# Kernel tuning notes

Hardware: AMD Instinct MI355X
Metric: run time of the kernel (lower is better)

Reference implementation:

```python
import jax, jax.numpy as jnp
import numpy as np

B, S, D, H = 2, 2048, 1024, 16
DK = D // H

def setup_inputs() -> dict:
    key = jax.random.key(0)
    ks = jax.random.split(key, 11)
    scale = 1.0 / np.sqrt(D)
    inp = {
        'q': jax.random.normal(ks[0], (B, S, D), jnp.float32),
        'k': jax.random.normal(ks[1], (B, S, D), jnp.float32),
        'v': jax.random.normal(ks[2], (B, S, D), jnp.float32),
        'Wq': jax.random.normal(ks[3], (D, D), jnp.float32) * scale,
        'bq': jnp.zeros((D,), jnp.float32),
        'Wk': jax.random.normal(ks[4], (D, D), jnp.float32) * scale,
        'bk': jnp.zeros((D,), jnp.float32),
        'Wv': jax.random.normal(ks[5], (D, D), jnp.float32) * scale,
        'bv': jnp.zeros((D,), jnp.float32),
        'Wo': jax.random.normal(ks[6], (D, D), jnp.float32) * scale,
        'bo': jnp.zeros((D,), jnp.float32),
    }
    return inp

def reference(q, k, v, Wq, bq, Wk, bk, Wv, bv, Wo, bo):
    # linear projections
    qp = q @ Wq + bq   # [B,S,D]
    kp = k @ Wk + bk
    vp = v @ Wv + bv
    # split heads -> [B,H,S,DK]
    qh = qp.reshape(B, S, H, DK).transpose(0, 2, 1, 3)
    kh = kp.reshape(B, S, H, DK).transpose(0, 2, 1, 3)
    vh = vp.reshape(B, S, H, DK).transpose(0, 2, 1, 3)
    scaled = jnp.einsum('bhqd,bhkd->bhqk', qh, kh) / jnp.sqrt(jnp.float32(DK))
    attn_score = jax.nn.softmax(scaled, axis=-1)  # [B,H,S,S]
    x = jnp.einsum('bhqk,bhkd->bhqd', attn_score, vh)
    # dropout is identity in eval mode
    out = x.transpose(0, 2, 1, 3).reshape(B, S, D)
    return (out @ Wo + bo, attn_score)
```

## Files before the change

kernel.cpp:

```cpp
#include <hip/hip_runtime.h>
#include <hip/hip_bf16.h>
#include <stdint.h>
#include <stddef.h>

typedef unsigned short u16;
typedef __attribute__((ext_vector_type(8))) short short8;
typedef __attribute__((ext_vector_type(4))) short bfx4;
typedef __attribute__((ext_vector_type(4))) float f32x4;
typedef __attribute__((ext_vector_type(4))) float f4;

constexpr int B_ = 2, S_ = 2048, D_ = 1024, H_ = 16;
constexpr size_t OUT_ELEMS = (size_t)B_ * S_ * D_;

__device__ __forceinline__ u16 f2bf(float f) {
    union { float f; unsigned u; } v; v.f = f;
    unsigned r = 0x7FFFu + ((v.u >> 16) & 1u);
    return (u16)((v.u + r) >> 16);
}

__device__ __forceinline__ void gload16(const void* g, void* l) {
    auto gg = reinterpret_cast<const __attribute__((address_space(1))) unsigned*>(
        reinterpret_cast<uintptr_t>(g));
    auto ll = reinterpret_cast<__attribute__((address_space(3))) unsigned*>(
        reinterpret_cast<uintptr_t>(l));
    __builtin_amdgcn_global_load_lds(gg, ll, 16, 0, 0);
}

__global__ __launch_bounds__(256) void wtrans_kernel(
    const float* __restrict__ W0, const float* __restrict__ W1,
    const float* __restrict__ W2, const float* __restrict__ W3,
    u16* __restrict__ T0, u16* __restrict__ T1, u16* __restrict__ T2, u16* __restrict__ T3)
{
    __shared__ __align__(16) u16 Ts[64][72];
    const float* W = blockIdx.z == 0 ? W0 : blockIdx.z == 1 ? W1 : blockIdx.z == 2 ? W2 : W3;
    u16*         T = blockIdx.z == 0 ? T0 : blockIdx.z == 1 ? T1 : blockIdx.z == 2 ? T2 : T3;
    const int t = threadIdx.x;
    const int r0 = blockIdx.y * 64, c0 = blockIdx.x * 64;
    const int row = t >> 2, qd = t & 3;

    const float* src = W + (size_t)(r0 + row) * 1024 + c0 + qd * 16;
    u16 tmp[16];
    #pragma unroll
    for (int j = 0; j < 16; j += 4) {
        f4 v = *(const f4*)(src + j);
        tmp[j] = f2bf(v[0]); tmp[j+1] = f2bf(v[1]); tmp[j+2] = f2bf(v[2]); tmp[j+3] = f2bf(v[3]);
    }
    #pragma unroll
    for (int j = 0; j < 16; j++) Ts[row][qd * 16 + j] = tmp[j];
    __syncthreads();
    short8 o0, o1;
    #pragma unroll
    for (int j = 0; j < 8; j++) { o0[j] = (short)Ts[qd*16 + j][row]; o1[j] = (short)Ts[qd*16 + 8 + j][row]; }
    u16* dst = T + (size_t)(c0 + row) * 1024 + r0 + qd * 16;
    *(short8*)dst = o0;
    *(short8*)(dst + 8) = o1;
}

__global__ __launch_bounds__(256) void vtrans_kernel(const u16* __restrict__ vp, u16* __restrict__ vt)
{
    __shared__ __align__(16) u16 Vs[64][72];
    const int t = threadIdx.x;
    const int s0 = blockIdx.x * 64;
    const int bh = blockIdx.y, b = bh >> 4, h = bh & 15;
    #pragma unroll
    for (int i = 0; i < 2; i++) {
        int c = t + 256 * i, row = c >> 3, ch = c & 7;
        *(short8*)(&Vs[row][ch * 8]) =
            *(const short8*)(vp + ((size_t)b * S_ + s0 + row) * D_ + h * 64 + ch * 8);
    }
    __syncthreads();
    #pragma unroll
    for (int i = 0; i < 2; i++) {
        int c = t + 256 * i, d = c >> 3, ch = c & 7;
        short8 o;
        #pragma unroll
        for (int j = 0; j < 8; j++) o[j] = (short)Vs[ch * 8 + j][d];
        *(short8*)(vt + ((size_t)bh * 64 + d) * S_ + s0 + ch * 8) = o;
    }
}

struct Stage { short8 h[2]; };

__device__ __forceinline__ void stage_load_f32(Stage& st, const float* Af, int row0, int K, int k0, int t) {
    const int row = t >> 1, half = t & 1;
    const float* p = Af + (size_t)(row0 + row) * K + k0 + half * 16;
    #pragma unroll
    for (int j = 0; j < 2; j++) {
        f4 v0 = *(const f4*)(p + j * 8);
        f4 v1 = *(const f4*)(p + j * 8 + 4);
        short8 hh;
        hh[0]=(short)f2bf(v0[0]); hh[1]=(short)f2bf(v0[1]); hh[2]=(short)f2bf(v0[2]); hh[3]=(short)f2bf(v0[3]);
        hh[4]=(short)f2bf(v1[0]); hh[5]=(short)f2bf(v1[1]); hh[6]=(short)f2bf(v1[2]); hh[7]=(short)f2bf(v1[3]);
        st.h[j] = hh;
    }
}

__device__ __forceinline__ void stage_store_f32(const Stage& st, u16* Ls, int t) {
    const int row = t >> 1, half = t & 1;
    #pragma unroll
    for (int j = 0; j < 2; j++) {
        int byteo = half * 32 + j * 16;
        *(short8*)((char*)Ls + row * 64 + (byteo ^ ((row & 3) << 4))) = st.h[j];
    }
}

template<int A_IS_F32, int OUT_IS_F32>
__global__ __launch_bounds__(256, 3)
void gemm_bt(const void* __restrict__ A0, const void* __restrict__ A1, const void* __restrict__ A2,
             const u16* __restrict__ Bt0, const u16* __restrict__ Bt1, const u16* __restrict__ Bt2,
             const float* __restrict__ bi0, const float* __restrict__ bi1, const float* __restrict__ bi2,
             void* __restrict__ C0, void* __restrict__ C1, void* __restrict__ C2,
             int M, int N, int K, float sc0, float sc1, float sc2)
{
    __shared__ __align__(16) u16 As[2][128 * 32];
    __shared__ __align__(16) u16 Bs[2][128 * 32];

    const int z = blockIdx.z;
    const void*  Aptr  = z == 0 ? A0  : z == 1 ? A1  : A2;
    const u16*   Bt    = z == 0 ? Bt0 : z == 1 ? Bt1 : Bt2;
    const float* bias  = z == 0 ? bi0 : z == 1 ? bi1 : bi2;
    void*        Cptr  = z == 0 ? C0  : z == 1 ? C1  : C2;
    const float  scale = z == 0 ? sc0 : z == 1 ? sc1 : sc2;

    const int t = threadIdx.x;
    const int w = t >> 6, l = t & 63, lr = l >> 4, lc = l & 15;
    const int wr = w >> 1, wc = w & 1;
    const int id = blockIdx.y * 8 + blockIdx.x;
    const int xcd = id & 7, i_ = id >> 3;
    const int row0 = ((xcd << 2) | ((i_ >> 4) << 1) | ((i_ >> 3) & 1)) * 128;
    const int col0 = (i_ & 7) * 128;
    const int NI = K >> 5;

    auto issueT = [&](const u16* P, int r0_, int i, u16* dst) {
        #pragma unroll
        for (int j = 0; j < 2; j++) {
            int off = j * 256 + t;
            int row = off >> 2, ch = off & 3;
            const char* src = (const char*)P + (((size_t)(r0_ + row) * K + i * 32) << 1)
                              + ((ch ^ (row & 3)) << 4);
            gload16(src, (char*)dst + off * 16);
        }
    };

    f32x4 acc[4][4] = {};
    Stage sa;
    issueT(Bt, col0, 0, Bs[0]);
    if constexpr (A_IS_F32) {
        stage_load_f32(sa, (const float*)Aptr, row0, K, 0, t);
        stage_store_f32(sa, As[0], t);
        stage_load_f32(sa, (const float*)Aptr, row0, K, 32, t);
    } else {
        issueT((const u16*)Aptr, row0, 0, As[0]);
    }
    __syncthreads();

    for (int i = 0; i < NI; i++) {
        const int p = i & 1;
        if (i + 1 < NI) {
            issueT(Bt, col0, i + 1, Bs[p ^ 1]);
            if constexpr (A_IS_F32) {
                stage_store_f32(sa, As[p ^ 1], t);
                const int kn = (i + 2 < NI) ? (i + 2) * 32 : 0;
                stage_load_f32(sa, (const float*)Aptr, row0, K, kn, t);
            } else {
                issueT((const u16*)Aptr, row0, i + 1, As[p ^ 1]);
            }
        }

        short8 af[4], bf_[4];
        #pragma unroll
        for (int mm = 0; mm < 4; mm++) {
            int r = wr * 64 + mm * 16 + lc;
            af[mm] = *(const short8*)((const char*)As[p] + r * 64 + ((lr * 16) ^ ((r & 3) << 4)));
        }
        #pragma unroll
        for (int nn = 0; nn < 4; nn++) {
            int r = wc * 64 + nn * 16 + lc;
            bf_[nn] = *(const short8*)((const char*)Bs[p] + r * 64 + ((lr * 16) ^ ((r & 3) << 4)));
        }
        #pragma unroll
        for (int mm = 0; mm < 4; mm++)
            #pragma unroll
            for (int nn = 0; nn < 4; nn++)
                acc[mm][nn] = __builtin_amdgcn_mfma_f32_16x16x32_bf16(af[mm], bf_[nn], acc[mm][nn], 0, 0, 0);
        __syncthreads();
    }

    float bv[4];
    #pragma unroll
    for (int nn = 0; nn < 4; nn++) bv[nn] = bias[col0 + wc * 64 + nn * 16 + lc];

    #pragma unroll
    for (int mm = 0; mm < 4; mm++) {
        const int row = row0 + wr * 64 + mm * 16 + lr * 4;
        #pragma unroll
        for (int nn = 0; nn < 4; nn++) {
            const int col = col0 + wc * 64 + nn * 16 + lc;
            #pragma unroll
            for (int r = 0; r < 4; r++) {
                float vv = (acc[mm][nn][r] + bv[nn]) * scale;
                if constexpr (OUT_IS_F32) ((float*)Cptr)[(size_t)(row + r) * N + col] = vv;
                else                      ((u16*) Cptr)[(size_t)(row + r) * N + col] = f2bf(vv);
            }
        }
    }
}

__global__ __launch_bounds__(512, 4)
void attn_kernel(const u16* __restrict__ qp, const u16* __restrict__ kp,
                 const u16* __restrict__ vt, float* __restrict__ Pout,
                 u16* __restrict__ xout)
{
    __shared__ __align__(16) u16 Qs[128 * 64];
    __shared__ __align__(16) u16 Ks[2][128 * 64];
    __shared__ __align__(16) u16 Vts[2][64 * 128];

    const int t = threadIdx.x;
    const int w = t >> 6, l = t & 63, lr = l >> 4, lc = l & 15;
    const int bid = blockIdx.x;
    const int s = ((bid & 7) << 6) | (bid >> 3);
    const int q0 = (s & 15) * 128;
    const int bh = s >> 4, b = bh >> 4, h = bh & 15;
    const float L2E = 1.4426950408889634f;
    constexpr int NT = S_ / 128;

    auto issueK = [&](int kt, int buf) {
        #pragma unroll
        for (int i = 0; i < 2; i++) {
            int off = i * 512 + t, row = off >> 3, ch = off & 7;
            const char* src = (const char*)kp + ((((size_t)b * S_ + kt * 128 + row) * D_ + h * 64) << 1)
                              + ((ch ^ (row & 7)) << 4);
            gload16(src, (char*)Ks[buf] + off * 16);
        }
    };
    auto issueV = [&](int kt, int buf) {
        #pragma unroll
        for (int i = 0; i < 2; i++) {
            int off = i * 512 + t, row = off >> 4, ch = off & 15;
            const char* src = (const char*)vt + ((((size_t)bh * 64 + row) * S_ + kt * 128) << 1)
                              + ((ch ^ (row & 7)) << 4);
            gload16(src, (char*)Vts[buf] + off * 16);
        }
    };

    issueK(0, 0);
    #pragma unroll
    for (int i = 0; i < 2; i++) {
        int c = t + 512 * i, row = c >> 3, ch = c & 7;
        short8 vq = *(const short8*)(qp + ((size_t)b * S_ + q0 + row) * D_ + h * 64 + ch * 8);
        *(short8*)((char*)Qs + row * 128 + ((ch * 16) ^ ((row & 7) << 4))) = vq;
    }
    __syncthreads();

    short8 qf[2];
    {
        int r = w * 16 + lc, sw = (r & 7) << 4;
        const char* qb = (const char*)Qs + r * 128;
        qf[0] = *(const short8*)(qb + ((lr * 16) ^ sw));
        qf[1] = *(const short8*)(qb + ((64 + lr * 16) ^ sw));
    }

    float sum = 0.f;
    for (int kt = 0; kt < NT; kt++) {
        const int p = kt & 1;
        if (kt + 1 < NT) issueK(kt + 1, p ^ 1);
        const char* Kb = (const char*)Ks[p];
        #pragma unroll
        for (int f = 0; f < 8; f++) {
            int r = f * 16 + lc, sw = (r & 7) << 4;
            const char* kb = Kb + r * 128;
            short8 k0 = *(const short8*)(kb + ((lr * 16) ^ sw));
            short8 k1 = *(const short8*)(kb + ((64 + lr * 16) ^ sw));
            f32x4 sacc = {};
            sacc = __builtin_amdgcn_mfma_f32_16x16x32_bf16(k0, qf[0], sacc, 0, 0, 0);
            sacc = __builtin_amdgcn_mfma_f32_16x16x32_bf16(k1, qf[1], sacc, 0, 0, 0);
            sum += exp2f(sacc[0] * L2E) + exp2f(sacc[1] * L2E)
                 + exp2f(sacc[2] * L2E) + exp2f(sacc[3] * L2E);
        }
        __syncthreads();
    }
    issueK(0, 0); issueV(0, 0);
    sum += __shfl_xor(sum, 16);
    sum += __shfl_xor(sum, 32);
    const float inv = 1.0f / sum;
    __syncthreads();

    f32x4 xacc[4] = {};
    float* pbase = Pout + ((size_t)bh * S_ + q0 + w * 16 + lc) * S_ + lr * 4;

    for (int kt = 0; kt < NT; kt++) {
        const int p = kt & 1;
        if (kt + 1 < NT) { issueK(kt + 1, p ^ 1); issueV(kt + 1, p ^ 1); }
        const char* Kb = (const char*)Ks[p];
        const char* Vb = (const char*)Vts[p];

        #pragma unroll
        for (int kk = 0; kk < 4; kk++) {
            union { unsigned u[4]; short8 s8; } pu;
            #pragma unroll
            for (int fo = 0; fo < 2; fo++) {
                const int f = kk * 2 + fo;
                int r = f * 16 + lc, sw = (r & 7) << 4;
                const char* kb = Kb + r * 128;
                short8 k0 = *(const short8*)(kb + ((lr * 16) ^ sw));
                short8 k1 = *(const short8*)(kb + ((64 + lr * 16) ^ sw));
                f32x4 sacc = {};
                sacc = __builtin_amdgcn_mfma_f32_16x16x32_bf16(k0, qf[0], sacc, 0, 0, 0);
                sacc = __builtin_amdgcn_mfma_f32_16x16x32_bf16(k1, qf[1], sacc, 0, 0, 0);
                f32x4 pv_;
                pv_[0] = exp2f(sacc[0] * L2E) * inv;
                pv_[1] = exp2f(sacc[1] * L2E) * inv;
                pv_[2] = exp2f(sacc[2] * L2E) * inv;
                pv_[3] = exp2f(sacc[3] * L2E) * inv;
                __builtin_nontemporal_store(pv_, (f32x4*)(pbase + (size_t)kt * 128 + f * 16));
                pu.u[fo * 2 + 0] = (unsigned)f2bf(pv_[0]) | ((unsigned)f2bf(pv_[1]) << 16);
                pu.u[fo * 2 + 1] = (unsigned)f2bf(pv_[2]) | ((unsigned)f2bf(pv_[3]) << 16);
            }
            const short8 pa = pu.s8;
            #pragma unroll
            for (int n = 0; n < 4; n++) {
                int rr = n * 16 + lc, sw2 = (rr & 7) << 4;
                const char* vrow = Vb + rr * 256;
                union { bfx4 h[2]; short8 s8; } vu;
                vu.h[0] = *(const bfx4*)(vrow + ((kk * 64 + lr * 8) ^ sw2));
                vu.h[1] = *(const bfx4*)(vrow + ((kk * 64 + 32 + lr * 8) ^ sw2));
                xacc[n] = __builtin_amdgcn_mfma_f32_16x16x32_bf16(pa, vu.s8, xacc[n], 0, 0, 0);
            }
        }
        __syncthreads();
    }

    #pragma unroll
    for (int n = 0; n < 4; n++) {
        #pragma unroll
        for (int r = 0; r < 4; r++) {
            int row = q0 + w * 16 + lr * 4 + r;
            int col = h * 64 + n * 16 + lc;
            xout[((size_t)b * S_ + row) * D_ + col] = f2bf(xacc[n][r]);
        }
    }
}

extern "C" void kernel_launch(void* const* d_in, const int* in_sizes, int n_in,
                              void* d_out, int out_size, void* d_ws, size_t ws_size,
                              hipStream_t stream)
{
    const float* qin = (const float*)d_in[0];
    const float* kin = (const float*)d_in[1];
    const float* vin = (const float*)d_in[2];
    const float* Wq  = (const float*)d_in[3];
    const float* bq  = (const float*)d_in[4];
    const float* Wk  = (const float*)d_in[5];
    const float* bk  = (const float*)d_in[6];
    const float* Wv  = (const float*)d_in[7];
    const float* bv  = (const float*)d_in[8];
    const float* Wo  = (const float*)d_in[9];
    const float* bo  = (const float*)d_in[10];

    u16* base = (u16*)d_ws;
    u16* Wqt = base;
    u16* Wkt = base + 1048576;
    u16* Wvt = base + 2097152;
    u16* Wot = base + 3145728;
    u16* qpb = base + 4194304;
    u16* kpb = base + 8388608;
    u16* vpb = base + 12582912;
    u16* vtb = base + 16777216;
    u16* xb  = base + 20971520;

    float* out  = (float*)d_out;
    float* Pout = out + OUT_ELEMS;

    const int M = B_ * S_;

    wtrans_kernel<<<dim3(16, 16, 4), 256, 0, stream>>>(Wq, Wk, Wv, Wo, Wqt, Wkt, Wvt, Wot);
    gemm_bt<1, 0><<<dim3(8, 32, 3), 256, 0, stream>>>(
        qin, kin, vin, Wqt, Wkt, Wvt, bq, bk, bv, qpb, kpb, vpb, M, D_, D_, 0.125f, 1.0f, 1.0f);
    vtrans_kernel<<<dim3(32, 32), 256, 0, stream>>>(vpb, vtb);
    attn_kernel<<<512, 512, 0, stream>>>(qpb, kpb, vtb, Pout, xb);
    gemm_bt<0, 1><<<dim3(8, 32, 1), 256, 0, stream>>>(
        xb, xb, xb, Wot, Wot, Wot, bo, bo, bo, out, out, out, M, D_, D_, 1.0f, 1.0f, 1.0f);
}
```

Baseline: 292.1 us.

## Pre-cast inputs to bf16 and replace syncthreads with explicit vmcnt waits

Adds a separate cast kernel that converts the fp32 q/k/v inputs to bf16 in workspace. The projection GEMM can then load A through async global-to-LDS copies instead of register staging with in-loop conversion. In both the GEMM and attention loops, full __syncthreads are replaced by explicit s_waitcnt vmcnt counts plus raw s_barrier, so the prefetch for the next tile stays in flight while the current one is consumed. The cost is an extra kernel launch and an extra round trip of q/k/v through memory, and the hand-counted vmcnt values must match the number of issued loads.

```diff
diff --git a/kernel.cpp b/kernel.cpp
--- a/kernel.cpp
+++ b/kernel.cpp
@@ -26,6 +26,27 @@
     __builtin_amdgcn_global_load_lds(gg, ll, 16, 0, 0);
 }
 
+#define VMWAIT(N) do { asm volatile("s_waitcnt vmcnt(" #N ")" ::: "memory"); } while (0)
+__device__ __forceinline__ void barrier_() {
+    __builtin_amdgcn_s_barrier();
+    __builtin_amdgcn_sched_barrier(0);
+}
+
+__global__ __launch_bounds__(256) void cast_kernel(
+    const float* __restrict__ q, const float* __restrict__ k, const float* __restrict__ v,
+    u16* __restrict__ qo, u16* __restrict__ ko, u16* __restrict__ vo)
+{
+    const float* src = blockIdx.z == 0 ? q : blockIdx.z == 1 ? k : v;
+    u16*         dst = blockIdx.z == 0 ? qo : blockIdx.z == 1 ? ko : vo;
+    size_t i = ((size_t)blockIdx.x * 256 + threadIdx.x) * 8;
+    f4 a = *(const f4*)(src + i);
+    f4 b = *(const f4*)(src + i + 4);
+    short8 o;
+    o[0]=(short)f2bf(a[0]); o[1]=(short)f2bf(a[1]); o[2]=(short)f2bf(a[2]); o[3]=(short)f2bf(a[3]);
+    o[4]=(short)f2bf(b[0]); o[5]=(short)f2bf(b[1]); o[6]=(short)f2bf(b[2]); o[7]=(short)f2bf(b[3]);
+    *(short8*)(dst + i) = o;
+}
+
 __global__ __launch_bounds__(256) void wtrans_kernel(
     const float* __restrict__ W0, const float* __restrict__ W1,
     const float* __restrict__ W2, const float* __restrict__ W3,
@@ -79,34 +100,9 @@
     }
 }
 
-struct Stage { short8 h[2]; };
-
-__device__ __forceinline__ void stage_load_f32(Stage& st, const float* Af, int row0, int K, int k0, int t) {
-    const int row = t >> 1, half = t & 1;
-    const float* p = Af + (size_t)(row0 + row) * K + k0 + half * 16;
-    #pragma unroll
-    for (int j = 0; j < 2; j++) {
-        f4 v0 = *(const f4*)(p + j * 8);
-        f4 v1 = *(const f4*)(p + j * 8 + 4);
-        short8 hh;
-        hh[0]=(short)f2bf(v0[0]); hh[1]=(short)f2bf(v0[1]); hh[2]=(short)f2bf(v0[2]); hh[3]=(short)f2bf(v0[3]);
-        hh[4]=(short)f2bf(v1[0]); hh[5]=(short)f2bf(v1[1]); hh[6]=(short)f2bf(v1[2]); hh[7]=(short)f2bf(v1[3]);
-        st.h[j] = hh;
-    }
-}
-
-__device__ __forceinline__ void stage_store_f32(const Stage& st, u16* Ls, int t) {
-    const int row = t >> 1, half = t & 1;
-    #pragma unroll
-    for (int j = 0; j < 2; j++) {
-        int byteo = half * 32 + j * 16;
-        *(short8*)((char*)Ls + row * 64 + (byteo ^ ((row & 3) << 4))) = st.h[j];
-    }
-}
-
-template<int A_IS_F32, int OUT_IS_F32>
+template<int OUT_IS_F32>
 __global__ __launch_bounds__(256, 3)
-void gemm_bt(const void* __restrict__ A0, const void* __restrict__ A1, const void* __restrict__ A2,
+void gemm_bt(const u16* __restrict__ A0, const u16* __restrict__ A1, const u16* __restrict__ A2,
              const u16* __restrict__ Bt0, const u16* __restrict__ Bt1, const u16* __restrict__ Bt2,
              const float* __restrict__ bi0, const float* __restrict__ bi1, const float* __restrict__ bi2,
              void* __restrict__ C0, void* __restrict__ C1, void* __restrict__ C2,
@@ -116,7 +112,7 @@
     __shared__ __align__(16) u16 Bs[2][128 * 32];
 
     const int z = blockIdx.z;
-    const void*  Aptr  = z == 0 ? A0  : z == 1 ? A1  : A2;
+    const u16*   Aptr  = z == 0 ? A0  : z == 1 ? A1  : A2;
     const u16*   Bt    = z == 0 ? Bt0 : z == 1 ? Bt1 : Bt2;
     const float* bias  = z == 0 ? bi0 : z == 1 ? bi1 : bi2;
     void*        Cptr  = z == 0 ? C0  : z == 1 ? C1  : C2;
@@ -143,29 +139,19 @@
     };
 
     f32x4 acc[4][4] = {};
-    Stage sa;
     issueT(Bt, col0, 0, Bs[0]);
-    if constexpr (A_IS_F32) {
-        stage_load_f32(sa, (const float*)Aptr, row0, K, 0, t);
-        stage_store_f32(sa, As[0], t);
-        stage_load_f32(sa, (const float*)Aptr, row0, K, 32, t);
-    } else {
-        issueT((const u16*)Aptr, row0, 0, As[0]);
-    }
-    __syncthreads();
+    issueT(Aptr, row0, 0, As[0]);
 
     for (int i = 0; i < NI; i++) {
         const int p = i & 1;
         if (i + 1 < NI) {
             issueT(Bt, col0, i + 1, Bs[p ^ 1]);
-            if constexpr (A_IS_F32) {
-                stage_store_f32(sa, As[p ^ 1], t);
-                const int kn = (i + 2 < NI) ? (i + 2) * 32 : 0;
-                stage_load_f32(sa, (const float*)Aptr, row0, K, kn, t);
-            } else {
-                issueT((const u16*)Aptr, row0, i + 1, As[p ^ 1]);
-            }
-        }
+            issueT(Aptr, row0, i + 1, As[p ^ 1]);
+            VMWAIT(4);
+        } else {
+            VMWAIT(0);
+        }
+        barrier_();
 
         short8 af[4], bf_[4];
         #pragma unroll
@@ -183,7 +169,7 @@
             #pragma unroll
             for (int nn = 0; nn < 4; nn++)
                 acc[mm][nn] = __builtin_amdgcn_mfma_f32_16x16x32_bf16(af[mm], bf_[nn], acc[mm][nn], 0, 0, 0);
-        __syncthreads();
+        __builtin_amdgcn_s_barrier();
     }
 
     float bv[4];
@@ -263,7 +249,9 @@
     float sum = 0.f;
     for (int kt = 0; kt < NT; kt++) {
         const int p = kt & 1;
-        if (kt + 1 < NT) issueK(kt + 1, p ^ 1);
+        if (kt + 1 < NT) { issueK(kt + 1, p ^ 1); VMWAIT(2); }
+        else             { VMWAIT(0); }
+        barrier_();
         const char* Kb = (const char*)Ks[p];
         #pragma unroll
         for (int f = 0; f < 8; f++) {
@@ -277,13 +265,12 @@
             sum += exp2f(sacc[0] * L2E) + exp2f(sacc[1] * L2E)
                  + exp2f(sacc[2] * L2E) + exp2f(sacc[3] * L2E);
         }
-        __syncthreads();
+        __builtin_amdgcn_s_barrier();
     }
     issueK(0, 0); issueV(0, 0);
     sum += __shfl_xor(sum, 16);
     sum += __shfl_xor(sum, 32);
     const float inv = 1.0f / sum;
-    __syncthreads();
 
     f32x4 xacc[4] = {};
     float* pbase = Pout + ((size_t)bh * S_ + q0 + w * 16 + lc) * S_ + lr * 4;
@@ -291,6 +278,10 @@
     for (int kt = 0; kt < NT; kt++) {
         const int p = kt & 1;
         if (kt + 1 < NT) { issueK(kt + 1, p ^ 1); issueV(kt + 1, p ^ 1); }
+        if (kt == 0)           VMWAIT(4);
+        else if (kt + 1 < NT)  VMWAIT(12);
+        else                   VMWAIT(8);
+        barrier_();
         const char* Kb = (const char*)Ks[p];
         const char* Vb = (const char*)Vts[p];
 
@@ -327,7 +318,7 @@
                 xacc[n] = __builtin_amdgcn_mfma_f32_16x16x32_bf16(pa, vu.s8, xacc[n], 0, 0, 0);
             }
         }
-        __syncthreads();
+        __builtin_amdgcn_s_barrier();
     }
 
     #pragma unroll
@@ -367,6 +358,9 @@
     u16* vpb = base + 12582912;
     u16* vtb = base + 16777216;
     u16* xb  = base + 20971520;
+    u16* qcb = base + 25165824;
+    u16* kcb = base + 29360128;
+    u16* vcb = base + 33554432;
 
     float* out  = (float*)d_out;
     float* Pout = out + OUT_ELEMS;
@@ -374,10 +368,11 @@
     const int M = B_ * S_;
 
     wtrans_kernel<<<dim3(16, 16, 4), 256, 0, stream>>>(Wq, Wk, Wv, Wo, Wqt, Wkt, Wvt, Wot);
-    gemm_bt<1, 0><<<dim3(8, 32, 3), 256, 0, stream>>>(
-        qin, kin, vin, Wqt, Wkt, Wvt, bq, bk, bv, qpb, kpb, vpb, M, D_, D_, 0.125f, 1.0f, 1.0f);
+    cast_kernel<<<dim3(2048, 1, 3), 256, 0, stream>>>(qin, kin, vin, qcb, kcb, vcb);
+    gemm_bt<0><<<dim3(8, 32, 3), 256, 0, stream>>>(
+        qcb, kcb, vcb, Wqt, Wkt, Wvt, bq, bk, bv, qpb, kpb, vpb, M, D_, D_, 0.125f, 1.0f, 1.0f);
     vtrans_kernel<<<dim3(32, 32), 256, 0, stream>>>(vpb, vtb);
     attn_kernel<<<512, 512, 0, stream>>>(qpb, kpb, vtb, Pout, xb);
-    gemm_bt<0, 1><<<dim3(8, 32, 1), 256, 0, stream>>>(
+    gemm_bt<1><<<dim3(8, 32, 1), 256, 0, stream>>>(
         xb, xb, xb, Wot, Wot, Wot, bo, bo, bo, out, out, out, M, D_, D_, 1.0f, 1.0f, 1.0f);
 }
```

New measurement: 282.3 us. 3.4% less time.
